# Kernel optimization log

Measured on AMD Instinct MI355X. Metric: run time of the kernel, lower is better.

Reference implementation:

```python
import jax, jax.numpy as jnp
import numpy as np

EQUATION = "bik,bkj->bij"  # matches init_kwargs


def setup_inputs() -> dict:
    key = jax.random.key(0)
    k0, k1 = jax.random.split(key)
    B, I, K, J = 32, 2048, 128, 2048
    input_0 = jax.random.normal(k0, (B, I, K), dtype=jnp.float32)
    input_1 = jax.random.normal(k1, (B, K, J), dtype=jnp.float32)
    return {"input_0": input_0, "input_1": input_1}


def reference(input_0, input_1):
    # Einsum module forward: binary contraction per the stored equation,
    # alpha=1, beta=0 (defaults in EinsumFunction when kwargs is empty).
    return jnp.einsum(EQUATION, input_0, input_1)
```

## Files before the change

### kernel.cpp

```cpp
#include <hip/hip_runtime.h>
#include <hip/hip_bf16.h>
#include <stdint.h>

#define B_DIM 32
#define I_DIM 2048
#define J_DIM 2048
#define K_DIM 128

typedef __attribute__((ext_vector_type(8))) short bf16x8;
typedef __attribute__((ext_vector_type(4))) short short4v;
typedef __attribute__((ext_vector_type(4))) float f32x4;

__device__ inline short f2bf(float f) {
  union { float f; uint32_t u; } v; v.f = f;
  uint32_t u = v.u + 0x7fffu + ((v.u >> 16) & 1u);
  return (short)(u >> 16);
}

__global__ __launch_bounds__(256) void convA_kernel(const float* __restrict__ A,
                                                    short* __restrict__ Ab) {
  const int idx = blockIdx.x * 256 + threadIdx.x;
  const float4* p = reinterpret_cast<const float4*>(A) + (size_t)idx * 2;
  const float4 a = p[0], b = p[1];
  bf16x8 o;
  o[0] = f2bf(a.x); o[1] = f2bf(a.y); o[2] = f2bf(a.z); o[3] = f2bf(a.w);
  o[4] = f2bf(b.x); o[5] = f2bf(b.y); o[6] = f2bf(b.z); o[7] = f2bf(b.w);
  reinterpret_cast<bf16x8*>(Ab)[idx] = o;
}

__global__ __launch_bounds__(256) void transB_kernel(const float* __restrict__ B,
                                                     short* __restrict__ Bt) {
  __shared__ __align__(16) short tile[64 * 128];
  const int t  = threadIdx.x;
  const int j0 = blockIdx.x * 64;
  const int b  = blockIdx.y;
  const float* Bb = B + (size_t)b * K_DIM * J_DIM;
  const int jj = t & 63, kq = t >> 6;
  #pragma unroll
  for (int kr = 0; kr < 32; ++kr) {
    const int k = kr * 4 + kq;
    const float v = Bb[(size_t)k * J_DIM + j0 + jj];
    tile[jj * 128 + (k ^ ((jj & 15) << 3))] = f2bf(v);
  }
  __syncthreads();
  short* Btb = Bt + (size_t)b * J_DIM * K_DIM;
  const int slot = t & 15, jr = t >> 4;
  #pragma unroll
  for (int r2 = 0; r2 < 4; ++r2) {
    const int j  = r2 * 16 + jr;
    const bf16x8 v = *reinterpret_cast<const bf16x8*>(&tile[j * 128 + slot * 8]);
    const int k0 = (slot * 8) ^ ((j & 15) << 3);
    *reinterpret_cast<bf16x8*>(Btb + (size_t)(j0 + j) * K_DIM + k0) = v;
  }
}

#define GLD_LDS16(g, l) __builtin_amdgcn_global_load_lds( \
    (const __attribute__((address_space(1))) uint32_t*)(g), \
    (__attribute__((address_space(3))) uint32_t*)(l), 16, 0, 0)

__global__ __launch_bounds__(256, 4) void gemm_kernel(const short* __restrict__ Ab,
                                                      const short* __restrict__ Bt,
                                                      float* __restrict__ C) {
  __shared__ __align__(16) short As[8192];
  __shared__ __align__(16) short Bs[8192];
  const int t = threadIdx.x;

  const int p   = blockIdx.x;
  const int lid = ((p & 7) << 10) | (p >> 3);
  const int jt  = lid & 15;
  const int it  = (lid >> 4) & 15;
  const int b   = lid >> 8;

  const int rsub  = t >> 3;
  const int kbyte = ((t & 7) << 4) ^ ((rsub & 7) << 4);
  const char* Asrc = (const char*)(Ab + (size_t)(b * I_DIM + it * 128 + rsub) * K_DIM) + kbyte;
  const char* Bsrc = (const char*)(Bt + (size_t)(b * J_DIM + jt * 128 + rsub) * K_DIM) + kbyte;
  char* Adst = (char*)As + (t >> 6) * 1024;
  char* Bdst = (char*)Bs + (t >> 6) * 1024;

  const int w = t >> 6, wm = w >> 1, wn = w & 1;
  const int lane = t & 63, lr = lane & 15, g = lane >> 4;
  const int swr = (lr & 7) << 4;

  f32x4 acc[4][4];
  #pragma unroll
  for (int m = 0; m < 4; ++m)
    #pragma unroll
    for (int n = 0; n < 4; ++n)
      acc[m][n] = (f32x4){0.f, 0.f, 0.f, 0.f};

  #pragma unroll
  for (int ki = 0; ki < 2; ++ki) {
    if (ki) __syncthreads();
    #pragma unroll
    for (int q = 0; q < 4; ++q) {
      GLD_LDS16(Asrc + q * 8192 + ki * 128, Adst + q * 4096);
      GLD_LDS16(Bsrc + q * 8192 + ki * 128, Bdst + q * 4096);
    }
    __syncthreads();
    #pragma unroll
    for (int kk = 0; kk < 2; ++kk) {
      bf16x8 af[4], bb[4];
      const int cb = kk * 64 + g * 16;
      #pragma unroll
      for (int m = 0; m < 4; ++m) {
        const int R = wm * 64 + m * 16 + lr;
        af[m] = *reinterpret_cast<const bf16x8*>((const char*)As + R * 128 + (cb ^ swr));
      }
      #pragma unroll
      for (int n = 0; n < 4; ++n) {
        const int R = wn * 64 + n * 16 + lr;
        bb[n] = *reinterpret_cast<const bf16x8*>((const char*)Bs + R * 128 + (cb ^ swr));
      }
      #pragma unroll
      for (int m = 0; m < 4; ++m)
        #pragma unroll
        for (int n = 0; n < 4; ++n)
          acc[m][n] = __builtin_amdgcn_mfma_f32_16x16x32_bf16(af[m], bb[n], acc[m][n], 0, 0, 0);
    }
  }

  float* Cb = C + (size_t)b * I_DIM * J_DIM;
  const int cbase = jt * 128 + wn * 64 + lr;
  #pragma unroll
  for (int m = 0; m < 4; ++m) {
    const int rbase = it * 128 + wm * 64 + m * 16 + g * 4;
    #pragma unroll
    for (int q = 0; q < 4; ++q) {
      float* crow = Cb + (size_t)(rbase + q) * J_DIM + cbase;
      #pragma unroll
      for (int n = 0; n < 4; ++n) crow[n * 16] = acc[m][n][q];
    }
  }
}

__device__ inline int swz_fb(int row, int kbyte) {
  return row * 128 + ((kbyte ^ ((row & 15) << 4)) >> 1);
}

__global__ __launch_bounds__(256, 2) void bmm_fallback(const float* __restrict__ A,
                                                       const float* __restrict__ Bm,
                                                       float* __restrict__ C) {
  __shared__ short As[128 * 128];
  __shared__ short Bs[128 * 128];
  const int t  = threadIdx.x;
  const int jt = blockIdx.x, it = blockIdx.y, b = blockIdx.z;
  const float* Abp = A  + (size_t)b * I_DIM * K_DIM;
  const float* Bbp = Bm + (size_t)b * K_DIM * J_DIM;
  {
    const int r0 = t >> 5;
    const int k0 = (t & 31) * 4;
    #pragma unroll 4
    for (int i8 = 0; i8 < 16; ++i8) {
      const int r = i8 * 8 + r0;
      const float4 v = *reinterpret_cast<const float4*>(
          Abp + (size_t)(it * 128 + r) * K_DIM + k0);
      short4v s; s.x = f2bf(v.x); s.y = f2bf(v.y); s.z = f2bf(v.z); s.w = f2bf(v.w);
      *reinterpret_cast<short4v*>(&As[swz_fb(r, 2 * k0)]) = s;
    }
  }
  {
    const int j  = t & 127;
    const int kq = (t >> 7) * 4;
    #pragma unroll 4
    for (int kb = 0; kb < 16; ++kb) {
      const int k0 = kb * 8 + kq;
      const float* p = Bbp + (size_t)k0 * J_DIM + jt * 128 + j;
      const float f0 = p[0], f1 = p[J_DIM], f2 = p[2 * J_DIM], f3 = p[3 * J_DIM];
      short4v s; s.x = f2bf(f0); s.y = f2bf(f1); s.z = f2bf(f2); s.w = f2bf(f3);
      *reinterpret_cast<short4v*>(&Bs[swz_fb(j, 2 * k0)]) = s;
    }
  }
  __syncthreads();
  const int w = t >> 6, wm = w >> 1, wn = w & 1;
  const int lane = t & 63, lr = lane & 15, g = lane >> 4;
  f32x4 acc[4][4];
  #pragma unroll
  for (int m = 0; m < 4; ++m)
    #pragma unroll
    for (int n = 0; n < 4; ++n) acc[m][n] = (f32x4){0.f, 0.f, 0.f, 0.f};
  #pragma unroll
  for (int kk = 0; kk < 4; ++kk) {
    bf16x8 af[4], bfr[4];
    const int kb = kk * 64 + g * 16;
    #pragma unroll
    for (int m = 0; m < 4; ++m) {
      const int r = wm * 64 + m * 16 + lr;
      af[m] = *reinterpret_cast<const bf16x8*>(&As[swz_fb(r, kb)]);
    }
    #pragma unroll
    for (int n = 0; n < 4; ++n) {
      const int r = wn * 64 + n * 16 + lr;
      bfr[n] = *reinterpret_cast<const bf16x8*>(&Bs[swz_fb(r, kb)]);
    }
    #pragma unroll
    for (int m = 0; m < 4; ++m)
      #pragma unroll
      for (int n = 0; n < 4; ++n)
        acc[m][n] = __builtin_amdgcn_mfma_f32_16x16x32_bf16(af[m], bfr[n], acc[m][n], 0, 0, 0);
  }
  float* Cb = C + (size_t)b * I_DIM * J_DIM;
  const int cbase = jt * 128 + wn * 64 + lr;
  #pragma unroll
  for (int m = 0; m < 4; ++m) {
    const int rbase = it * 128 + wm * 64 + m * 16 + g * 4;
    #pragma unroll
    for (int q = 0; q < 4; ++q) {
      float* crow = Cb + (size_t)(rbase + q) * J_DIM + cbase;
      #pragma unroll
      for (int n = 0; n < 4; ++n) crow[n * 16] = acc[m][n][q];
    }
  }
}

extern "C" void kernel_launch(void* const* d_in, const int* in_sizes, int n_in,
                              void* d_out, int out_size, void* d_ws, size_t ws_size,
                              hipStream_t stream) {
  const float* A  = (const float*)d_in[0];
  const float* Bm = (const float*)d_in[1];
  float* C = (float*)d_out;
  const size_t needA = (size_t)B_DIM * I_DIM * K_DIM * sizeof(short);
  const size_t needB = (size_t)B_DIM * K_DIM * J_DIM * sizeof(short);
  if (ws_size >= needA + needB) {
    short* Ab = (short*)d_ws;
    short* Bt = (short*)((char*)d_ws + needA);
    convA_kernel<<<4096, 256, 0, stream>>>(A, Ab);
    transB_kernel<<<dim3(J_DIM / 64, B_DIM), 256, 0, stream>>>(Bm, Bt);
    gemm_kernel<<<8192, 256, 0, stream>>>(Ab, Bt, C);
  } else {
    bmm_fallback<<<dim3(J_DIM / 128, I_DIM / 128, B_DIM), 256, 0, stream>>>(A, Bm, C);
  }
}
```

Measured before the change: 147.5 us.

## Switch GEMM to 32x32x16 MFMA, vectorize B transpose loads, drop block swizzle

The GEMM kernel now uses 32x32x16 bf16 MFMA with 2x2 accumulator tiles per wave instead of 4x4 tiles of 16x16x32, changing the LDS fragment addressing and the output store pattern. The B transpose kernel reads float4 vectors along J instead of scalars. The block-index remapping that interleaved blocks across batches is removed in favor of linear ordering. These aim to cut LDS reads per MFMA and global load instruction count, at the risk of worse cache or XCD locality and of LDS bank conflicts on the transpose writes.

```diff
diff --git a/kernel.cpp b/kernel.cpp
--- a/kernel.cpp
+++ b/kernel.cpp
@@ -10,6 +10,7 @@
 typedef __attribute__((ext_vector_type(8))) short bf16x8;
 typedef __attribute__((ext_vector_type(4))) short short4v;
 typedef __attribute__((ext_vector_type(4))) float f32x4;
+typedef __attribute__((ext_vector_type(16))) float f32x16;
 
 __device__ inline short f2bf(float f) {
   union { float f; uint32_t u; } v; v.f = f;
@@ -20,11 +21,11 @@
 __global__ __launch_bounds__(256) void convA_kernel(const float* __restrict__ A,
                                                     short* __restrict__ Ab) {
   const int idx = blockIdx.x * 256 + threadIdx.x;
-  const float4* p = reinterpret_cast<const float4*>(A) + (size_t)idx * 2;
-  const float4 a = p[0], b = p[1];
+  const f32x4* p = reinterpret_cast<const f32x4*>(A) + (size_t)idx * 2;
+  const f32x4 a = p[0], b = p[1];
   bf16x8 o;
-  o[0] = f2bf(a.x); o[1] = f2bf(a.y); o[2] = f2bf(a.z); o[3] = f2bf(a.w);
-  o[4] = f2bf(b.x); o[5] = f2bf(b.y); o[6] = f2bf(b.z); o[7] = f2bf(b.w);
+  o[0] = f2bf(a[0]); o[1] = f2bf(a[1]); o[2] = f2bf(a[2]); o[3] = f2bf(a[3]);
+  o[4] = f2bf(b[0]); o[5] = f2bf(b[1]); o[6] = f2bf(b[2]); o[7] = f2bf(b[3]);
   reinterpret_cast<bf16x8*>(Ab)[idx] = o;
 }
 
@@ -35,12 +36,17 @@
   const int j0 = blockIdx.x * 64;
   const int b  = blockIdx.y;
   const float* Bb = B + (size_t)b * K_DIM * J_DIM;
-  const int jj = t & 63, kq = t >> 6;
-  #pragma unroll
-  for (int kr = 0; kr < 32; ++kr) {
-    const int k = kr * 4 + kq;
-    const float v = Bb[(size_t)k * J_DIM + j0 + jj];
-    tile[jj * 128 + (k ^ ((jj & 15) << 3))] = f2bf(v);
+  const int qj = t & 15;
+  const int k0 = t >> 4;
+  #pragma unroll
+  for (int kp = 0; kp < 8; ++kp) {
+    const int k = kp * 16 + k0;
+    const f32x4 v = *reinterpret_cast<const f32x4*>(Bb + (size_t)k * J_DIM + j0 + 4 * qj);
+    #pragma unroll
+    for (int e = 0; e < 4; ++e) {
+      const int jj = 4 * qj + e;
+      tile[jj * 128 + (k ^ ((jj & 15) << 3))] = f2bf(v[e]);
+    }
   }
   __syncthreads();
   short* Btb = Bt + (size_t)b * J_DIM * K_DIM;
@@ -49,8 +55,8 @@
   for (int r2 = 0; r2 < 4; ++r2) {
     const int j  = r2 * 16 + jr;
     const bf16x8 v = *reinterpret_cast<const bf16x8*>(&tile[j * 128 + slot * 8]);
-    const int k0 = (slot * 8) ^ ((j & 15) << 3);
-    *reinterpret_cast<bf16x8*>(Btb + (size_t)(j0 + j) * K_DIM + k0) = v;
+    const int kk0 = (slot * 8) ^ ((j & 15) << 3);
+    *reinterpret_cast<bf16x8*>(Btb + (size_t)(j0 + j) * K_DIM + kk0) = v;
   }
 }
 
@@ -64,12 +70,8 @@
   __shared__ __align__(16) short As[8192];
   __shared__ __align__(16) short Bs[8192];
   const int t = threadIdx.x;
-
-  const int p   = blockIdx.x;
-  const int lid = ((p & 7) << 10) | (p >> 3);
-  const int jt  = lid & 15;
-  const int it  = (lid >> 4) & 15;
-  const int b   = lid >> 8;
+  const int p = blockIdx.x;
+  const int jt = p & 15, it = (p >> 4) & 15, b = p >> 8;
 
   const int rsub  = t >> 3;
   const int kbyte = ((t & 7) << 4) ^ ((rsub & 7) << 4);
@@ -78,16 +80,18 @@
   char* Adst = (char*)As + (t >> 6) * 1024;
   char* Bdst = (char*)Bs + (t >> 6) * 1024;
 
-  const int w = t >> 6, wm = w >> 1, wn = w & 1;
-  const int lane = t & 63, lr = lane & 15, g = lane >> 4;
-  const int swr = (lr & 7) << 4;
-
-  f32x4 acc[4][4];
-  #pragma unroll
-  for (int m = 0; m < 4; ++m)
-    #pragma unroll
-    for (int n = 0; n < 4; ++n)
-      acc[m][n] = (f32x4){0.f, 0.f, 0.f, 0.f};
+  const int w  = t >> 6, wm = w >> 1, wn = w & 1;
+  const int l  = t & 63;
+  const int lr32 = l & 31;
+  const int g2   = l >> 5;
+
+  f32x16 acc[2][2];
+  #pragma unroll
+  for (int m = 0; m < 2; ++m)
+    #pragma unroll
+    for (int n = 0; n < 2; ++n)
+      #pragma unroll
+      for (int e = 0; e < 16; ++e) acc[m][n][e] = 0.f;
 
   #pragma unroll
   for (int ki = 0; ki < 2; ++ki) {
@@ -99,37 +103,39 @@
     }
     __syncthreads();
     #pragma unroll
-    for (int kk = 0; kk < 2; ++kk) {
-      bf16x8 af[4], bb[4];
-      const int cb = kk * 64 + g * 16;
-      #pragma unroll
-      for (int m = 0; m < 4; ++m) {
-        const int R = wm * 64 + m * 16 + lr;
-        af[m] = *reinterpret_cast<const bf16x8*>((const char*)As + R * 128 + (cb ^ swr));
+    for (int kq = 0; kq < 4; ++kq) {
+      const int s = kq * 2 + g2;
+      bf16x8 af[2], bb[2];
+      #pragma unroll
+      for (int m = 0; m < 2; ++m) {
+        const int R = wm * 64 + m * 32 + lr32;
+        af[m] = *reinterpret_cast<const bf16x8*>((const char*)As + R * 128 + ((s ^ (R & 7)) << 4));
       }
       #pragma unroll
-      for (int n = 0; n < 4; ++n) {
-        const int R = wn * 64 + n * 16 + lr;
-        bb[n] = *reinterpret_cast<const bf16x8*>((const char*)Bs + R * 128 + (cb ^ swr));
+      for (int n = 0; n < 2; ++n) {
+        const int R = wn * 64 + n * 32 + lr32;
+        bb[n] = *reinterpret_cast<const bf16x8*>((const char*)Bs + R * 128 + ((s ^ (R & 7)) << 4));
       }
       #pragma unroll
-      for (int m = 0; m < 4; ++m)
+      for (int m = 0; m < 2; ++m)
         #pragma unroll
-        for (int n = 0; n < 4; ++n)
-          acc[m][n] = __builtin_amdgcn_mfma_f32_16x16x32_bf16(af[m], bb[n], acc[m][n], 0, 0, 0);
+        for (int n = 0; n < 2; ++n)
+          acc[m][n] = __builtin_amdgcn_mfma_f32_32x32x16_bf16(af[m], bb[n], acc[m][n], 0, 0, 0);
     }
   }
 
   float* Cb = C + (size_t)b * I_DIM * J_DIM;
-  const int cbase = jt * 128 + wn * 64 + lr;
-  #pragma unroll
-  for (int m = 0; m < 4; ++m) {
-    const int rbase = it * 128 + wm * 64 + m * 16 + g * 4;
-    #pragma unroll
-    for (int q = 0; q < 4; ++q) {
-      float* crow = Cb + (size_t)(rbase + q) * J_DIM + cbase;
-      #pragma unroll
-      for (int n = 0; n < 4; ++n) crow[n * 16] = acc[m][n][q];
+  #pragma unroll
+  for (int m = 0; m < 2; ++m) {
+    const int rowbase = it * 128 + wm * 64 + m * 32 + 4 * g2;
+    #pragma unroll
+    for (int n = 0; n < 2; ++n) {
+      const int colbase = jt * 128 + wn * 64 + n * 32 + lr32;
+      #pragma unroll
+      for (int r = 0; r < 16; ++r) {
+        const int row = rowbase + (r & 3) + 8 * (r >> 2);
+        Cb[(size_t)row * J_DIM + colbase] = acc[m][n][r];
+      }
     }
   }
 }
```

After: 157.3 us. 6.6% more time.
